# Optimization experiments

Hardware: AMD Instinct MI355X
Metric: run time of the kernel (lower is better)

## Reference

```python
import jax, jax.numpy as jnp
import numpy as np

D_MODEL = 2048
NUM_HEADS = 16
HEAD_DIM = D_MODEL // NUM_HEADS
ENTROPY_THRESHOLD = 0.01
B, T = 4, 2048


def setup_inputs() -> dict:
    key = jax.random.key(0)
    ks = jax.random.split(key, 10)
    s = 1.0 / np.sqrt(D_MODEL)
    inp = {
        "x": jax.random.normal(ks[0], (B, T, D_MODEL), dtype=jnp.float32),
        "mask": jnp.ones((B, T), dtype=jnp.int32),
        "Wq": jax.random.uniform(ks[1], (D_MODEL, D_MODEL), jnp.float32, -s, s),
        "bq": jax.random.uniform(ks[2], (D_MODEL,), jnp.float32, -s, s),
        "Wk": jax.random.uniform(ks[3], (D_MODEL, D_MODEL), jnp.float32, -s, s),
        "bk": jax.random.uniform(ks[4], (D_MODEL,), jnp.float32, -s, s),
        "Wv": jax.random.uniform(ks[5], (D_MODEL, D_MODEL), jnp.float32, -s, s),
        "bv": jax.random.uniform(ks[6], (D_MODEL,), jnp.float32, -s, s),
        "Wo": jax.random.uniform(ks[7], (D_MODEL, D_MODEL), jnp.float32, -s, s),
        "bo": jax.random.uniform(ks[8], (D_MODEL,), jnp.float32, -s, s),
    }
    return inp


def reference(x, mask, Wq, bq, Wk, bk, Wv, bv, Wo, bo):
    Bx, Tx, C = x.shape

    def heads(y):  # (B,T,C) -> (B,H,T,hd)
        return y.reshape(Bx, Tx, NUM_HEADS, HEAD_DIM).transpose(0, 2, 1, 3)

    q = heads(x @ Wq.T + bq)
    k = heads(x @ Wk.T + bk)
    v = heads(x @ Wv.T + bv)

    scores = jnp.einsum("bhqd,bhkd->bhqk", q, k) / np.sqrt(HEAD_DIM).astype(np.float32)
    scores = jnp.where(mask[:, None, None, :] == 0, -jnp.inf, scores)
    weights = jax.nn.softmax(scores, axis=-1)

    # entropy reduction (eval mode: conditional dropout is identity, so ent
    # does not alter the output, but we compute it faithfully)
    ent = -jnp.sum(weights * jnp.log(weights + 1e-9), axis=-1).mean()
    weights = jnp.where(ent < ENTROPY_THRESHOLD, weights, weights)  # dropout(p=0.1, training=False) == identity

    attended = jnp.einsum("bhqk,bhkd->bhqd", weights, v)
    attended = attended.transpose(0, 2, 1, 3).reshape(Bx, Tx, C)
    return attended @ Wo.T + bo
```

## Files before the change

### kernel.cpp

```cpp
#include <hip/hip_runtime.h>
#include <cstdint>
#include <cstddef>

#define D_MODEL 2048
#define T_SEQ   2048
#define N_BATCH 4
#define N_HEAD  16
#define HD      128
#define M_ROWS  (N_BATCH * T_SEQ)
#define N_QKV   (3 * D_MODEL)

typedef short          s8x  __attribute__((ext_vector_type(8)));
typedef float          f4x  __attribute__((ext_vector_type(4)));
typedef float          f4v  __attribute__((ext_vector_type(4)));
typedef unsigned short u16;
typedef u16            u16x8 __attribute__((ext_vector_type(8)));

__device__ __forceinline__ u16 f2bf(float f) {
    union { float f; unsigned u; } v; v.f = f;
    unsigned r = (v.u + 0x7FFFu + ((v.u >> 16) & 1u)) >> 16;
    return (u16)r;
}

__device__ __forceinline__ void glds16(const void* g, void* l) {
    __builtin_amdgcn_global_load_lds(
        (const __attribute__((address_space(1))) void*)g,
        (__attribute__((address_space(3))) void*)l, 16, 0, 0);
}

template<int CTRL>
__device__ __forceinline__ float dppror(float v) {
    int i = __builtin_bit_cast(int, v);
    int r = __builtin_amdgcn_update_dpp(i, i, CTRL, 0xf, 0xf, true);
    return __builtin_bit_cast(float, r);
}
__device__ __forceinline__ float rowmax16(float v) {
    v = fmaxf(v, dppror<0x128>(v));
    v = fmaxf(v, dppror<0x124>(v));
    v = fmaxf(v, dppror<0x122>(v));
    v = fmaxf(v, dppror<0x121>(v));
    return v;
}

__global__ void cvt_f32_bf16(const float* __restrict__ in, u16* __restrict__ out, int n8) {
    int i = blockIdx.x * blockDim.x + threadIdx.x;
    int stride = gridDim.x * blockDim.x;
    for (; i < n8; i += stride) {
        f4v a = reinterpret_cast<const f4v*>(in)[2 * i];
        f4v b = reinterpret_cast<const f4v*>(in)[2 * i + 1];
        u16x8 o;
        o[0] = f2bf(a[0]); o[1] = f2bf(a[1]); o[2] = f2bf(a[2]); o[3] = f2bf(a[3]);
        o[4] = f2bf(b[0]); o[5] = f2bf(b[1]); o[6] = f2bf(b[2]); o[7] = f2bf(b[3]);
        reinterpret_cast<u16x8*>(out)[i] = o;
    }
}

template<bool OUT_BF16>
__global__ __launch_bounds__(256)
void gemm_bt(const u16* __restrict__ A, const u16* __restrict__ B,
             const float* __restrict__ bias, void* __restrict__ C,
             int M, int N, int K, int nbn, float qscale, int qcols) {
    __shared__ u16 As[128 * 32];
    __shared__ u16 Bs[128 * 32];

    int nwg = gridDim.x;
    int wg  = blockIdx.x;
    int qx  = nwg >> 3;
    wg = (wg & 7) * qx + (wg >> 3);
    int bm = wg / nbn, bn = wg % nbn;

    int t   = threadIdx.x;
    int wid = t >> 6;
    int l15 = t & 15, l4 = (t >> 4) & 3;
    int wr  = wid >> 1, wc = wid & 1;

    f4x acc[4][4] = {};

    const u16* ga = A + (size_t)(bm * 128 + (t >> 2)) * K + (t & 3) * 8;
    const u16* gb = B + (size_t)(bn * 128 + (t >> 2)) * K + (t & 3) * 8;
    char* lA = (char*)As + wid * 1024;
    char* lB = (char*)Bs + wid * 1024;

    for (int k0 = 0; k0 < K; k0 += 32) {
        glds16(ga,              lA);
        glds16(ga + 64 * (size_t)K, lA + 4096);
        glds16(gb,              lB);
        glds16(gb + 64 * (size_t)K, lB + 4096);
        ga += 32; gb += 32;
        __syncthreads();

        s8x af[4], bfr[4];
        #pragma unroll
        for (int m = 0; m < 4; m++) {
            af[m]  = *reinterpret_cast<const s8x*>(As + (wr * 64 + m * 16 + l15) * 32 + l4 * 8);
            bfr[m] = *reinterpret_cast<const s8x*>(Bs + (wc * 64 + m * 16 + l15) * 32 + l4 * 8);
        }
        #pragma unroll
        for (int m = 0; m < 4; m++)
            #pragma unroll
            for (int n = 0; n < 4; n++)
                acc[m][n] = __builtin_amdgcn_mfma_f32_16x16x32_bf16(af[m], bfr[n], acc[m][n], 0, 0, 0);
        __syncthreads();
    }

    int row0 = bm * 128 + wr * 64;
    int col0 = bn * 128 + wc * 64;
    #pragma unroll
    for (int n = 0; n < 4; n++) {
        int col = col0 + n * 16 + l15;
        float bv = bias[col];
        float sc = (col < qcols) ? qscale : 1.0f;
        #pragma unroll
        for (int m = 0; m < 4; m++) {
            #pragma unroll
            for (int r = 0; r < 4; r++) {
                int row = row0 + m * 16 + l4 * 4 + r;
                float v = (acc[m][n][r] + bv) * sc;
                if (OUT_BF16) ((u16*)C)[(size_t)row * N + col]   = f2bf(v);
                else          ((float*)C)[(size_t)row * N + col] = v;
            }
        }
    }
}

__global__ __launch_bounds__(256, 2)
void attn(const u16* __restrict__ qkv, const int* __restrict__ mask,
          u16* __restrict__ att) {
    __shared__ u16  Vt[128 * 64];
    __shared__ u16  Pl[4][32 * 64];
    __shared__ float mbuf[2][64];

    int wg = blockIdx.x;
    int q8 = gridDim.x >> 3;
    wg = (wg & 7) * q8 + (wg >> 3);
    int bh = wg >> 4;
    int qb = wg & 15;
    int b  = bh >> 4, h = bh & 15;

    int t = threadIdx.x, wid = t >> 6;
    int lane = t & 63, l15 = lane & 15, l4 = lane >> 4;

    const size_t rs = N_QKV;
    const u16* qbase = qkv + (size_t)(b * T_SEQ) * rs;
    const u16* kbase = qbase + D_MODEL + h * HD;
    const u16* vbase = qbase + 2 * D_MODEL + h * HD;

    s8x qf[2][4];
    #pragma unroll
    for (int ms = 0; ms < 2; ms++)
        #pragma unroll
        for (int kk = 0; kk < 4; kk++) {
            int row = qb * 128 + wid * 32 + ms * 16 + l15;
            qf[ms][kk] = *reinterpret_cast<const s8x*>(
                qbase + (size_t)row * rs + h * HD + kk * 32 + l4 * 8);
        }

    f4x acc[2][8] = {};
    float mrun[2][4], lrun[2][4];
    #pragma unroll
    for (int ms = 0; ms < 2; ms++)
        #pragma unroll
        for (int r = 0; r < 4; r++) { mrun[ms][r] = -__builtin_inff(); lrun[ms][r] = 0.f; }

    int vp = t & 31;
    int vs = t >> 5;
    u16* Pw = Pl[wid];

    {
        s8x v0a = *reinterpret_cast<const s8x*>(vbase + (size_t)(2 * vp) * rs + vs * 16);
        s8x v0b = *reinterpret_cast<const s8x*>(vbase + (size_t)(2 * vp) * rs + vs * 16 + 8);
        s8x v1a = *reinterpret_cast<const s8x*>(vbase + (size_t)(2 * vp + 1) * rs + vs * 16);
        s8x v1b = *reinterpret_cast<const s8x*>(vbase + (size_t)(2 * vp + 1) * rs + vs * 16 + 8);
        if (t < 64) mbuf[0][t] = mask[b * T_SEQ + t] ? 0.f : -__builtin_inff();
        #pragma unroll
        for (int j = 0; j < 8; j++) {
            int r0 = vs * 16 + j, r1 = vs * 16 + 8 + j;
            unsigned w0 = (u16)v0a[j] | ((unsigned)(u16)v1a[j] << 16);
            unsigned w1 = (u16)v0b[j] | ((unsigned)(u16)v1b[j] << 16);
            *reinterpret_cast<unsigned*>(&Vt[r0 * 64 + (((vp >> 2) ^ (r0 & 7)) << 3) + (vp & 3) * 2]) = w0;
            *reinterpret_cast<unsigned*>(&Vt[r1 * 64 + (((vp >> 2) ^ (r1 & 7)) << 3) + (vp & 3) * 2]) = w1;
        }
    }

    for (int tt = 0; tt < T_SEQ / 64; tt++) {
        int kv0 = tt * 64;
        int cur = tt & 1, nxt = cur ^ 1;
        int kvn = kv0 + 64; if (kvn >= T_SEQ) kvn = 0;

        s8x v0a = *reinterpret_cast<const s8x*>(vbase + (size_t)(kvn + 2 * vp) * rs + vs * 16);
        s8x v0b = *reinterpret_cast<const s8x*>(vbase + (size_t)(kvn + 2 * vp) * rs + vs * 16 + 8);
        s8x v1a = *reinterpret_cast<const s8x*>(vbase + (size_t)(kvn + 2 * vp + 1) * rs + vs * 16);
        s8x v1b = *reinterpret_cast<const s8x*>(vbase + (size_t)(kvn + 2 * vp + 1) * rs + vs * 16 + 8);

        f4x sf[2][4] = {};
        #pragma unroll
        for (int t4 = 0; t4 < 4; t4++) {
            s8x kf[4];
            #pragma unroll
            for (int kk = 0; kk < 4; kk++)
                kf[kk] = *reinterpret_cast<const s8x*>(
                    kbase + (size_t)(kv0 + t4 * 16 + l15) * rs + kk * 32 + l4 * 8);
            #pragma unroll
            for (int ms = 0; ms < 2; ms++)
                #pragma unroll
                for (int kk = 0; kk < 4; kk++)
                    sf[ms][t4] = __builtin_amdgcn_mfma_f32_16x16x32_bf16(qf[ms][kk], kf[kk], sf[ms][t4], 0, 0, 0);
        }

        __syncthreads();

        float mbv[4];
        #pragma unroll
        for (int t4 = 0; t4 < 4; t4++) mbv[t4] = mbuf[cur][t4 * 16 + l15];
        #pragma unroll
        for (int ms = 0; ms < 2; ms++)
            #pragma unroll
            for (int t4 = 0; t4 < 4; t4++)
                sf[ms][t4] += mbv[t4];

        #pragma unroll
        for (int ms = 0; ms < 2; ms++) {
            float mx[4];
            #pragma unroll
            for (int r = 0; r < 4; r++) {
                float a0 = fmaxf(fmaxf(sf[ms][0][r], sf[ms][1][r]),
                                 fmaxf(sf[ms][2][r], sf[ms][3][r]));
                mx[r] = rowmax16(a0);
            }
            bool grow = false;
            #pragma unroll
            for (int r = 0; r < 4; r++) grow |= (mx[r] > mrun[ms][r] + 8.f);
            if (__any(grow)) {
                f4x fv;
                #pragma unroll
                for (int r = 0; r < 4; r++) {
                    float mn = fmaxf(mrun[ms][r], mx[r]);
                    fv[r] = exp2f(mrun[ms][r] - mn);
                    mrun[ms][r] = mn;
                    lrun[ms][r] *= fv[r];
                }
                #pragma unroll
                for (int dt = 0; dt < 8; dt++) acc[ms][dt] *= fv;
            }
            #pragma unroll
            for (int t4 = 0; t4 < 4; t4++) {
                int pslot = (t4 << 1) + (l15 >> 3);
                #pragma unroll
                for (int r = 0; r < 4; r++) {
                    float p = exp2f(sf[ms][t4][r] - mrun[ms][r]);
                    lrun[ms][r] += p;
                    int prow = ms * 16 + l4 * 4 + r;
                    Pw[prow * 64 + ((pslot ^ (prow & 7)) << 3) + (l15 & 7)] = f2bf(p);
                }
            }
        }
        asm volatile("" ::: "memory");

        s8x pa[2][2];
        #pragma unroll
        for (int ms = 0; ms < 2; ms++)
            #pragma unroll
            for (int ks = 0; ks < 2; ks++) {
                int prow = ms * 16 + l15;
                pa[ms][ks] = *reinterpret_cast<const s8x*>(
                    Pw + prow * 64 + ((((ks << 2) + l4) ^ (prow & 7)) << 3));
            }
        #pragma unroll
        for (int dt = 0; dt < 8; dt++) {
            int vrow = dt * 16 + l15;
            s8x vbf[2];
            #pragma unroll
            for (int ks = 0; ks < 2; ks++)
                vbf[ks] = *reinterpret_cast<const s8x*>(
                    &Vt[vrow * 64 + ((((ks << 2) + l4) ^ (vrow & 7)) << 3)]);
            #pragma unroll
            for (int ms = 0; ms < 2; ms++)
                #pragma unroll
                for (int ks = 0; ks < 2; ks++)
                    acc[ms][dt] = __builtin_amdgcn_mfma_f32_16x16x32_bf16(pa[ms][ks], vbf[ks], acc[ms][dt], 0, 0, 0);
        }

        __syncthreads();

        if (t < 64) mbuf[nxt][t] = mask[b * T_SEQ + kvn + t] ? 0.f : -__builtin_inff();
        #pragma unroll
        for (int j = 0; j < 8; j++) {
            int r0 = vs * 16 + j, r1 = vs * 16 + 8 + j;
            unsigned w0 = (u16)v0a[j] | ((unsigned)(u16)v1a[j] << 16);
            unsigned w1 = (u16)v0b[j] | ((unsigned)(u16)v1b[j] << 16);
            *reinterpret_cast<unsigned*>(&Vt[r0 * 64 + (((vp >> 2) ^ (r0 & 7)) << 3) + (vp & 3) * 2]) = w0;
            *reinterpret_cast<unsigned*>(&Vt[r1 * 64 + (((vp >> 2) ^ (r1 & 7)) << 3) + (vp & 3) * 2]) = w1;
        }
    }

    #pragma unroll
    for (int ms = 0; ms < 2; ms++) {
        f4x inv;
        #pragma unroll
        for (int r = 0; r < 4; r++) {
            float s = lrun[ms][r];
            #pragma unroll
            for (int sh = 1; sh <= 8; sh <<= 1) s += __shfl_xor(s, sh);
            inv[r] = 1.f / s;
        }
        #pragma unroll
        for (int dt = 0; dt < 8; dt++) {
            f4x o = acc[ms][dt] * inv;
            #pragma unroll
            for (int r = 0; r < 4; r++) {
                int row = qb * 128 + wid * 32 + ms * 16 + l4 * 4 + r;
                int col = h * HD + dt * 16 + l15;
                att[(size_t)(b * T_SEQ + row) * D_MODEL + col] = f2bf(o[r]);
            }
        }
    }
}

extern "C" void kernel_launch(void* const* d_in, const int* in_sizes, int n_in,
                              void* d_out, int out_size, void* d_ws, size_t ws_size,
                              hipStream_t stream) {
    (void)in_sizes; (void)n_in; (void)out_size; (void)ws_size;

    const float* x    = (const float*)d_in[0];
    const int*   mask = (const int*)d_in[1];
    const float* Wq   = (const float*)d_in[2];
    const float* bq   = (const float*)d_in[3];
    const float* Wk   = (const float*)d_in[4];
    const float* bk   = (const float*)d_in[5];
    const float* Wv   = (const float*)d_in[6];
    const float* bv   = (const float*)d_in[7];
    const float* Wo   = (const float*)d_in[8];
    const float* bo   = (const float*)d_in[9];
    float* out = (float*)d_out;

    char* ws = (char*)d_ws;
    u16*   xb   = (u16*)(ws);
    u16*   wqkv = (u16*)(ws + 33554432);
    u16*   wo   = (u16*)(ws + 58720256);
    float* bqkv = (float*)(ws + 67108864);
    u16*   qkvb = (u16*)(ws + 67133440);
    u16*   attb = (u16*)(ws + 167796736);

    cvt_f32_bf16<<<2048, 256, 0, stream>>>(x,  xb,               16777216 / 8);
    cvt_f32_bf16<<<1024, 256, 0, stream>>>(Wq, wqkv,              4194304 / 8);
    cvt_f32_bf16<<<1024, 256, 0, stream>>>(Wk, wqkv + 4194304,    4194304 / 8);
    cvt_f32_bf16<<<1024, 256, 0, stream>>>(Wv, wqkv + 8388608,    4194304 / 8);
    cvt_f32_bf16<<<1024, 256, 0, stream>>>(Wo, wo,                4194304 / 8);
    hipMemcpyAsync(bqkv,        bq, 2048 * 4, hipMemcpyDeviceToDevice, stream);
    hipMemcpyAsync(bqkv + 2048, bk, 2048 * 4, hipMemcpyDeviceToDevice, stream);
    hipMemcpyAsync(bqkv + 4096, bv, 2048 * 4, hipMemcpyDeviceToDevice, stream);

    const float cs = 0.08838834764831845f * 1.4426950408889634f;

    gemm_bt<true><<<64 * 48, 256, 0, stream>>>(xb, wqkv, bqkv, qkvb, M_ROWS, N_QKV, D_MODEL, 48, cs, D_MODEL);
    attn<<<1024, 256, 0, stream>>>(qkvb, mask, attb);
    gemm_bt<false><<<64 * 16, 256, 0, stream>>>(attb, wo, bo, out, M_ROWS, D_MODEL, D_MODEL, 16, 1.0f, 0);
}
```

Baseline: 901.5 us.

## Switch attention to 32x32x16 MFMA with transposed S and register-resident P

Rewrites the attention inner loop around 32x32x16 bf16 MFMAs. It computes S transposed (K as the A operand), so each lane owns one query column and the row max and sum need only a single cross-half shuffle. P is converted in registers with packed bf16 conversion and a permlane32 swap, which removes the per-wave P staging through shared memory and the DPP row reductions. The additive -inf mask becomes a multiplicative 0/1 mask that is skipped when a ballot shows the whole tile is unmasked. This adds cross-lane shuffles when rescaling and normalizing, and relies on gfx950-specific instructions.

```diff
diff --git a/kernel.cpp b/kernel.cpp
--- a/kernel.cpp
+++ b/kernel.cpp
@@ -10,9 +10,10 @@
 #define M_ROWS  (N_BATCH * T_SEQ)
 #define N_QKV   (3 * D_MODEL)
 
-typedef short          s8x  __attribute__((ext_vector_type(8)));
-typedef float          f4x  __attribute__((ext_vector_type(4)));
-typedef float          f4v  __attribute__((ext_vector_type(4)));
+typedef short          s8x   __attribute__((ext_vector_type(8)));
+typedef float          f4x   __attribute__((ext_vector_type(4)));
+typedef float          f16x  __attribute__((ext_vector_type(16)));
+typedef float          f4v   __attribute__((ext_vector_type(4)));
 typedef unsigned short u16;
 typedef u16            u16x8 __attribute__((ext_vector_type(8)));
 
@@ -22,24 +23,19 @@
     return (u16)r;
 }
 
+__device__ __forceinline__ unsigned pkbf(float lo, float hi) {
+    unsigned r;
+    asm("v_cvt_pk_bf16_f32 %0, %1, %2" : "=v"(r) : "v"(lo), "v"(hi));
+    return r;
+}
+__device__ __forceinline__ void pl32swap(unsigned& a, unsigned& b) {
+    asm volatile("v_permlane32_swap_b32 %0, %1" : "+v"(a), "+v"(b));
+}
+
 __device__ __forceinline__ void glds16(const void* g, void* l) {
     __builtin_amdgcn_global_load_lds(
         (const __attribute__((address_space(1))) void*)g,
         (__attribute__((address_space(3))) void*)l, 16, 0, 0);
-}
-
-template<int CTRL>
-__device__ __forceinline__ float dppror(float v) {
-    int i = __builtin_bit_cast(int, v);
-    int r = __builtin_amdgcn_update_dpp(i, i, CTRL, 0xf, 0xf, true);
-    return __builtin_bit_cast(float, r);
-}
-__device__ __forceinline__ float rowmax16(float v) {
-    v = fmaxf(v, dppror<0x128>(v));
-    v = fmaxf(v, dppror<0x124>(v));
-    v = fmaxf(v, dppror<0x122>(v));
-    v = fmaxf(v, dppror<0x121>(v));
-    return v;
 }
 
 __global__ void cvt_f32_bf16(const float* __restrict__ in, u16* __restrict__ out, int n8) {
@@ -126,9 +122,9 @@
 __global__ __launch_bounds__(256, 2)
 void attn(const u16* __restrict__ qkv, const int* __restrict__ mask,
           u16* __restrict__ att) {
-    __shared__ u16  Vt[128 * 64];
-    __shared__ u16  Pl[4][32 * 64];
+    __shared__ u16   Vt[128 * 64];
     __shared__ float mbuf[2][64];
+    __shared__ int   mflag[2];
 
     int wg = blockIdx.x;
     int q8 = gridDim.x >> 3;
@@ -138,40 +134,37 @@
     int b  = bh >> 4, h = bh & 15;
 
     int t = threadIdx.x, wid = t >> 6;
-    int lane = t & 63, l15 = lane & 15, l4 = lane >> 4;
+    int lane = t & 63, l31 = lane & 31, hi = lane >> 5;
 
     const size_t rs = N_QKV;
     const u16* qbase = qkv + (size_t)(b * T_SEQ) * rs;
     const u16* kbase = qbase + D_MODEL + h * HD;
     const u16* vbase = qbase + 2 * D_MODEL + h * HD;
 
-    s8x qf[2][4];
+    int qrow = qb * 128 + wid * 32 + l31;
+    s8x qf[8];
     #pragma unroll
-    for (int ms = 0; ms < 2; ms++)
-        #pragma unroll
-        for (int kk = 0; kk < 4; kk++) {
-            int row = qb * 128 + wid * 32 + ms * 16 + l15;
-            qf[ms][kk] = *reinterpret_cast<const s8x*>(
-                qbase + (size_t)row * rs + h * HD + kk * 32 + l4 * 8);
-        }
-
-    f4x acc[2][8] = {};
-    float mrun[2][4], lrun[2][4];
-    #pragma unroll
-    for (int ms = 0; ms < 2; ms++)
-        #pragma unroll
-        for (int r = 0; r < 4; r++) { mrun[ms][r] = -__builtin_inff(); lrun[ms][r] = 0.f; }
+    for (int ks = 0; ks < 8; ks++)
+        qf[ks] = *reinterpret_cast<const s8x*>(
+            qbase + (size_t)qrow * rs + h * HD + ks * 16 + hi * 8);
+
+    f16x oacc[4] = {};
+    float mrun = -__builtin_inff(), lrun = 0.f;
 
     int vp = t & 31;
     int vs = t >> 5;
-    u16* Pw = Pl[wid];
 
     {
         s8x v0a = *reinterpret_cast<const s8x*>(vbase + (size_t)(2 * vp) * rs + vs * 16);
         s8x v0b = *reinterpret_cast<const s8x*>(vbase + (size_t)(2 * vp) * rs + vs * 16 + 8);
         s8x v1a = *reinterpret_cast<const s8x*>(vbase + (size_t)(2 * vp + 1) * rs + vs * 16);
         s8x v1b = *reinterpret_cast<const s8x*>(vbase + (size_t)(2 * vp + 1) * rs + vs * 16 + 8);
-        if (t < 64) mbuf[0][t] = mask[b * T_SEQ + t] ? 0.f : -__builtin_inff();
+        if (wid == 0) {
+            int mv = mask[b * T_SEQ + t] != 0;
+            mbuf[0][t] = mv ? 1.f : 0.f;
+            unsigned long long bl = __ballot(mv);
+            if (t == 0) mflag[0] = (bl == ~0ull);
+        }
         #pragma unroll
         for (int j = 0; j < 8; j++) {
             int r0 = vs * 16 + j, r1 = vs * 16 + 8 + j;
@@ -192,97 +185,113 @@
         s8x v1a = *reinterpret_cast<const s8x*>(vbase + (size_t)(kvn + 2 * vp + 1) * rs + vs * 16);
         s8x v1b = *reinterpret_cast<const s8x*>(vbase + (size_t)(kvn + 2 * vp + 1) * rs + vs * 16 + 8);
 
-        f4x sf[2][4] = {};
-        #pragma unroll
-        for (int t4 = 0; t4 < 4; t4++) {
-            s8x kf[4];
-            #pragma unroll
-            for (int kk = 0; kk < 4; kk++)
-                kf[kk] = *reinterpret_cast<const s8x*>(
-                    kbase + (size_t)(kv0 + t4 * 16 + l15) * rs + kk * 32 + l4 * 8);
-            #pragma unroll
-            for (int ms = 0; ms < 2; ms++)
+        f16x sf0 = {}, sf1 = {};
+        #pragma unroll
+        for (int ks = 0; ks < 8; ks++) {
+            s8x k0 = *reinterpret_cast<const s8x*>(
+                kbase + (size_t)(kv0 + l31) * rs + ks * 16 + hi * 8);
+            s8x k1 = *reinterpret_cast<const s8x*>(
+                kbase + (size_t)(kv0 + 32 + l31) * rs + ks * 16 + hi * 8);
+            sf0 = __builtin_amdgcn_mfma_f32_32x32x16_bf16(k0, qf[ks], sf0, 0, 0, 0);
+            sf1 = __builtin_amdgcn_mfma_f32_32x32x16_bf16(k1, qf[ks], sf1, 0, 0, 0);
+        }
+
+        __syncthreads();
+
+        bool allone = mflag[cur] != 0;
+
+        float a0 = sf0[0], a1 = sf0[1], a2 = sf0[2], a3 = sf0[3];
+        #pragma unroll
+        for (int r = 4; r < 16; r += 4) {
+            a0 = fmaxf(a0, sf0[r]);     a1 = fmaxf(a1, sf0[r + 1]);
+            a2 = fmaxf(a2, sf0[r + 2]); a3 = fmaxf(a3, sf0[r + 3]);
+        }
+        #pragma unroll
+        for (int r = 0; r < 16; r += 4) {
+            a0 = fmaxf(a0, sf1[r]);     a1 = fmaxf(a1, sf1[r + 1]);
+            a2 = fmaxf(a2, sf1[r + 2]); a3 = fmaxf(a3, sf1[r + 3]);
+        }
+        float mx = fmaxf(fmaxf(a0, a1), fmaxf(a2, a3));
+        mx = fmaxf(mx, __shfl_xor(mx, 32));
+
+        if (__any(mx > mrun + 8.f)) {
+            float mn = fmaxf(mx, mrun);
+            float f  = __builtin_amdgcn_exp2f(mrun - mn);
+            mrun = mn;
+            lrun *= f;
+            float fq[16];
+            #pragma unroll
+            for (int r = 0; r < 16; r++)
+                fq[r] = __shfl(f, (r & 3) + 8 * (r >> 2) + 4 * hi);
+            #pragma unroll
+            for (int db = 0; db < 4; db++)
                 #pragma unroll
-                for (int kk = 0; kk < 4; kk++)
-                    sf[ms][t4] = __builtin_amdgcn_mfma_f32_16x16x32_bf16(qf[ms][kk], kf[kk], sf[ms][t4], 0, 0, 0);
+                for (int r = 0; r < 16; r++)
+                    oacc[db][r] *= fq[r];
+        }
+
+        float p0[16], p1[16];
+        #pragma unroll
+        for (int r = 0; r < 16; r++) {
+            p0[r] = __builtin_amdgcn_exp2f(sf0[r] - mrun);
+            p1[r] = __builtin_amdgcn_exp2f(sf1[r] - mrun);
+        }
+        if (!allone) {
+            #pragma unroll
+            for (int g = 0; g < 4; g++) {
+                f4v m0 = *reinterpret_cast<const f4v*>(&mbuf[cur][8 * g + 4 * hi]);
+                f4v m1 = *reinterpret_cast<const f4v*>(&mbuf[cur][32 + 8 * g + 4 * hi]);
+                #pragma unroll
+                for (int c = 0; c < 4; c++) { p0[4 * g + c] *= m0[c]; p1[4 * g + c] *= m1[c]; }
+            }
+        }
+        {
+            float t0 = 0, t1 = 0, t2 = 0, t3 = 0;
+            #pragma unroll
+            for (int r = 0; r < 16; r += 4) {
+                t0 += p0[r];     t1 += p0[r + 1]; t2 += p0[r + 2]; t3 += p0[r + 3];
+                t0 += p1[r];     t1 += p1[r + 1]; t2 += p1[r + 2]; t3 += p1[r + 3];
+            }
+            lrun += (t0 + t1) + (t2 + t3);
+        }
+
+        union { unsigned w[4]; s8x v; } paf[4];
+        #pragma unroll
+        for (int bb = 0; bb < 2; bb++) {
+            float* pp = bb ? p1 : p0;
+            #pragma unroll
+            for (int s2 = 0; s2 < 2; s2++) {
+                unsigned P0 = pkbf(pp[8 * s2 + 0], pp[8 * s2 + 1]);
+                unsigned P1 = pkbf(pp[8 * s2 + 2], pp[8 * s2 + 3]);
+                unsigned P2 = pkbf(pp[8 * s2 + 4], pp[8 * s2 + 5]);
+                unsigned P3 = pkbf(pp[8 * s2 + 6], pp[8 * s2 + 7]);
+                pl32swap(P0, P2);
+                pl32swap(P1, P3);
+                int s = 2 * bb + s2;
+                paf[s].w[0] = P0; paf[s].w[1] = P1;
+                paf[s].w[2] = P2; paf[s].w[3] = P3;
+            }
+        }
+
+        #pragma unroll
+        for (int db = 0; db < 4; db++) {
+            int vrow = db * 32 + l31;
+            #pragma unroll
+            for (int s = 0; s < 4; s++) {
+                int slot = ((s << 1) + hi) ^ (vrow & 7);
+                s8x vb = *reinterpret_cast<const s8x*>(&Vt[vrow * 64 + slot * 8]);
+                oacc[db] = __builtin_amdgcn_mfma_f32_32x32x16_bf16(paf[s].v, vb, oacc[db], 0, 0, 0);
+            }
         }
 
         __syncthreads();
 
-        float mbv[4];
-        #pragma unroll
-        for (int t4 = 0; t4 < 4; t4++) mbv[t4] = mbuf[cur][t4 * 16 + l15];
-        #pragma unroll
-        for (int ms = 0; ms < 2; ms++)
-            #pragma unroll
-            for (int t4 = 0; t4 < 4; t4++)
-                sf[ms][t4] += mbv[t4];
-
-        #pragma unroll
-        for (int ms = 0; ms < 2; ms++) {
-            float mx[4];
-            #pragma unroll
-            for (int r = 0; r < 4; r++) {
-                float a0 = fmaxf(fmaxf(sf[ms][0][r], sf[ms][1][r]),
-                                 fmaxf(sf[ms][2][r], sf[ms][3][r]));
-                mx[r] = rowmax16(a0);
-            }
-            bool grow = false;
-            #pragma unroll
-            for (int r = 0; r < 4; r++) grow |= (mx[r] > mrun[ms][r] + 8.f);
-            if (__any(grow)) {
-                f4x fv;
-                #pragma unroll
-                for (int r = 0; r < 4; r++) {
-                    float mn = fmaxf(mrun[ms][r], mx[r]);
-                    fv[r] = exp2f(mrun[ms][r] - mn);
-                    mrun[ms][r] = mn;
-                    lrun[ms][r] *= fv[r];
-                }
-                #pragma unroll
-                for (int dt = 0; dt < 8; dt++) acc[ms][dt] *= fv;
-            }
-            #pragma unroll
-            for (int t4 = 0; t4 < 4; t4++) {
-                int pslot = (t4 << 1) + (l15 >> 3);
-                #pragma unroll
-                for (int r = 0; r < 4; r++) {
-                    float p = exp2f(sf[ms][t4][r] - mrun[ms][r]);
-                    lrun[ms][r] += p;
-                    int prow = ms * 16 + l4 * 4 + r;
-                    Pw[prow * 64 + ((pslot ^ (prow & 7)) << 3) + (l15 & 7)] = f2bf(p);
-                }
-            }
-        }
-        asm volatile("" ::: "memory");
-
-        s8x pa[2][2];
-        #pragma unroll
-        for (int ms = 0; ms < 2; ms++)
-            #pragma unroll
-            for (int ks = 0; ks < 2; ks++) {
-                int prow = ms * 16 + l15;
-                pa[ms][ks] = *reinterpret_cast<const s8x*>(
-                    Pw + prow * 64 + ((((ks << 2) + l4) ^ (prow & 7)) << 3));
-            }
-        #pragma unroll
-        for (int dt = 0; dt < 8; dt++) {
-            int vrow = dt * 16 + l15;
-            s8x vbf[2];
-            #pragma unroll
-            for (int ks = 0; ks < 2; ks++)
-                vbf[ks] = *reinterpret_cast<const s8x*>(
-                    &Vt[vrow * 64 + ((((ks << 2) + l4) ^ (vrow & 7)) << 3)]);
-            #pragma unroll
-            for (int ms = 0; ms < 2; ms++)
-                #pragma unroll
-                for (int ks = 0; ks < 2; ks++)
-                    acc[ms][dt] = __builtin_amdgcn_mfma_f32_16x16x32_bf16(pa[ms][ks], vbf[ks], acc[ms][dt], 0, 0, 0);
-        }
-
-        __syncthreads();
-
-        if (t < 64) mbuf[nxt][t] = mask[b * T_SEQ + kvn + t] ? 0.f : -__builtin_inff();
+        if (wid == 0) {
+            int mv = mask[b * T_SEQ + kvn + t] != 0;
+            mbuf[nxt][t] = mv ? 1.f : 0.f;
+            unsigned long long bl = __ballot(mv);
+            if (t == 0) mflag[nxt] = (bl == ~0ull);
+        }
         #pragma unroll
         for (int j = 0; j < 8; j++) {
             int r0 = vs * 16 + j, r1 = vs * 16 + 8 + j;
@@ -293,25 +302,19 @@
         }
     }
 
+    lrun += __shfl_xor(lrun, 32);
+    float inv = 1.f / lrun;
+    float invq[16];
     #pragma unroll
-    for (int ms = 0; ms < 2; ms++) {
-        f4x inv;
-        #pragma unroll
-        for (int r = 0; r < 4; r++) {
-            float s = lrun[ms][r];
-            #pragma unroll
-            for (int sh = 1; sh <= 8; sh <<= 1) s += __shfl_xor(s, sh);
-            inv[r] = 1.f / s;
-        }
-        #pragma unroll
-        for (int dt = 0; dt < 8; dt++) {
-            f4x o = acc[ms][dt] * inv;
-            #pragma unroll
-            for (int r = 0; r < 4; r++) {
-                int row = qb * 128 + wid * 32 + ms * 16 + l4 * 4 + r;
-                int col = h * HD + dt * 16 + l15;
-                att[(size_t)(b * T_SEQ + row) * D_MODEL + col] = f2bf(o[r]);
-            }
+    for (int r = 0; r < 16; r++)
+        invq[r] = __shfl(inv, (r & 3) + 8 * (r >> 2) + 4 * hi);
+    #pragma unroll
+    for (int db = 0; db < 4; db++) {
+        #pragma unroll
+        for (int r = 0; r < 16; r++) {
+            int row = qb * 128 + wid * 32 + (r & 3) + 8 * (r >> 2) + 4 * hi;
+            int col = h * HD + db * 32 + l31;
+            att[(size_t)(b * T_SEQ + row) * D_MODEL + col] = f2bf(oacc[db][r] * invq[r]);
         }
     }
 }
```

After: 853.8 us. 5.3% less time.
